# Performance work log

Hardware: AMD Instinct MI355X
Metric: run time of the kernel (lower is better)

Reference implementation:

```python
import jax, jax.numpy as jnp
import numpy as np

N_CODES = 1024
DIM = 64
COMMITMENT = 0.25


def setup_inputs() -> dict:
    key = jax.random.key(0)
    k1, k2 = jax.random.split(key)
    z = jax.random.normal(k1, (32, DIM, 64, 64), dtype=jnp.float32)  # [B, C, H, W]
    codebook = jax.random.uniform(
        k2, (N_CODES, DIM), dtype=jnp.float32,
        minval=-1.0 / N_CODES, maxval=1.0 / N_CODES,
    )
    return {"z": z, "codebook": codebook}


def reference(z, codebook):
    B, C, H, W = z.shape
    # [B, C, H, W] -> [B*H*W, C]
    z_flat = jnp.transpose(z, (0, 2, 3, 1)).reshape(-1, C)
    # Pairwise squared distances: ||z||^2 + ||e||^2 - 2 z.e  -> [N, n_codes]
    dists = (
        jnp.sum(z_flat * z_flat, axis=1, keepdims=True)
        + jnp.sum(codebook * codebook, axis=1)
        - 2.0 * (z_flat @ codebook.T)
    )
    indices = jnp.argmin(dists, axis=1)  # [N]
    z_q = codebook[indices].reshape(B, H, W, C).transpose(0, 3, 1, 2)  # [B, C, H, W]

    commit_loss = jnp.mean((jax.lax.stop_gradient(z_q) - z) ** 2)
    codebook_loss = jnp.mean((z_q - jax.lax.stop_gradient(z)) ** 2)
    vq_loss = codebook_loss + COMMITMENT * commit_loss

    # Straight-through estimator
    z_q_st = z + jax.lax.stop_gradient(z_q - z)

    # Codebook usage fraction (jit-friendly equivalent of len(unique)/n_codes)
    counts = jnp.zeros((codebook.shape[0],), dtype=jnp.int32).at[indices].add(1)
    usage = jnp.mean((counts > 0).astype(jnp.float32))

    return z_q_st, vq_loss, usage, indices.reshape(B, H, W)
```

## Files before the change

kernel.cpp:

```cpp
#include <hip/hip_runtime.h>

#define NCODES 1024
#define DIM 64
#define HW 4096
#define CHW 262144
#define NPOS 131072
#define NELEM 8388608
#define TAU 4e-5f

#define WS_LOSS 0
#define WS_CNT 4
#define WS_FLAGS 256
#define WS_BSWZ 8192
#define WS_CBN 270336
#define WS_LIST 274432

typedef __attribute__((ext_vector_type(8))) short bf16x8;
typedef __attribute__((ext_vector_type(4))) float f32x4;
typedef __attribute__((ext_vector_type(4))) unsigned int u32x4;

__device__ __forceinline__ unsigned short f2bf(float x) {
  unsigned u = __float_as_uint(x);
  return (unsigned short)((u + 0x7FFFu + ((u >> 16) & 1u)) >> 16);
}
__device__ __forceinline__ float bf2f(unsigned short h) {
  return __uint_as_float(((unsigned)h) << 16);
}
__device__ __forceinline__ unsigned fxf(float d) {
  unsigned u = __float_as_uint(d);
  return (u & 0x80000000u) ? ~u : (u | 0x80000000u);
}

__global__ __launch_bounds__(256) void vq_prep(const float* __restrict__ cb,
                                               unsigned short* __restrict__ bswz,
                                               float* __restrict__ cbn) {
  int t = blockIdx.x * 256 + threadIdx.x;
  int n = t >> 6, k = t & 63;
  float v = cb[n * 64 + k];
  unsigned short h = f2bf(v);
  unsigned short lo = f2bf(v - bf2f(h));
  int i = n >> 4, lmod = n & 15;
  int q = k >> 5, kr = k & 31;
  int e = ((kr >> 4) << 2) | (kr & 3);
  int l = lmod | (((kr >> 2) & 3) << 4);
  bswz[(((i * 2 + 0) * 2 + q) * 64 + l) * 8 + e] = h;
  bswz[(((i * 2 + 1) * 2 + q) * 64 + l) * 8 + e] = lo;
  if (k == 0) {
    const float* ep = cb + n * 64;
    float s = 0.f;
#pragma unroll
    for (int c = 0; c < 64; ++c) s = fmaf(ep[c], ep[c], s);
    cbn[n] = s;
  }
}

__global__ __launch_bounds__(512, 4) void vq_phaseA(
    const float* __restrict__ z, const float* __restrict__ cb,
    const unsigned short* __restrict__ bswz, const float* __restrict__ cbn,
    float* __restrict__ out_zq, float* __restrict__ out_idx,
    float* __restrict__ loss, unsigned* __restrict__ cnt,
    unsigned* __restrict__ list, int* __restrict__ flags) {
  const int tid = threadIdx.x, w = tid >> 6, l = tid & 63;
  const int l15 = l & 15, lg = (l >> 4) & 3;
  const int posbase = blockIdx.x * 256;
  const int b = posbase >> 12;
  const int hwb = posbase & 4095;

  bf16x8 A[2][2][2];
#pragma unroll
  for (int s = 0; s < 2; ++s) {
    const float* zp = z + (size_t)b * CHW + (hwb + w * 32 + s * 16 + l15);
#pragma unroll
    for (int q = 0; q < 2; ++q) {
      bf16x8 ah, al;
#pragma unroll
      for (int e = 0; e < 8; ++e) {
        int c = q * 32 + ((e >> 2) << 4) + (lg << 2) + (e & 3);
        float v = zp[c * HW];
        unsigned short h = f2bf(v);
        ah[e] = (short)h;
        al[e] = (short)f2bf(v - bf2f(h));
      }
      A[s][q][0] = ah;
      A[s][q][1] = al;
    }
  }

  float bd[2][4], b2[2][4];
  unsigned bi[2][4];
#pragma unroll
  for (int s = 0; s < 2; ++s)
#pragma unroll
    for (int r = 0; r < 4; ++r) {
      bd[s][r] = 3.4e38f; b2[s][r] = 3.4e38f; bi[s][r] = 0;
    }

  const u32x4* B = (const u32x4*)bswz;
  for (int i = 0; i < 64; ++i) {
    bf16x8 b00 = __builtin_bit_cast(bf16x8, B[(i * 4 + 0) * 64 + l]);
    bf16x8 b01 = __builtin_bit_cast(bf16x8, B[(i * 4 + 1) * 64 + l]);
    bf16x8 b10 = __builtin_bit_cast(bf16x8, B[(i * 4 + 2) * 64 + l]);
    bf16x8 b11 = __builtin_bit_cast(bf16x8, B[(i * 4 + 3) * 64 + l]);
    float cbnv = cbn[i * 16 + l15];
    unsigned nb = (unsigned)(i * 16 + l15);
#pragma unroll
    for (int s = 0; s < 2; ++s) {
      f32x4 C = {0.f, 0.f, 0.f, 0.f};
      C = __builtin_amdgcn_mfma_f32_16x16x32_bf16(A[s][0][0], b00, C, 0, 0, 0);
      C = __builtin_amdgcn_mfma_f32_16x16x32_bf16(A[s][1][0], b01, C, 0, 0, 0);
      C = __builtin_amdgcn_mfma_f32_16x16x32_bf16(A[s][0][0], b10, C, 0, 0, 0);
      C = __builtin_amdgcn_mfma_f32_16x16x32_bf16(A[s][1][0], b11, C, 0, 0, 0);
      C = __builtin_amdgcn_mfma_f32_16x16x32_bf16(A[s][0][1], b00, C, 0, 0, 0);
      C = __builtin_amdgcn_mfma_f32_16x16x32_bf16(A[s][1][1], b01, C, 0, 0, 0);
#pragma unroll
      for (int r = 0; r < 4; ++r) {
        float d = fmaf(C[r], -2.0f, cbnv);
        bool lt = d < bd[s][r];
        float loser = lt ? bd[s][r] : d;
        b2[s][r] = fminf(b2[s][r], loser);
        bd[s][r] = fminf(bd[s][r], d);
        bi[s][r] = lt ? nb : bi[s][r];
      }
    }
  }

  __shared__ unsigned res[256];
#pragma unroll
  for (int s = 0; s < 2; ++s)
#pragma unroll
    for (int r = 0; r < 4; ++r) {
      float d = bd[s][r], s2 = b2[s][r];
      unsigned idx = bi[s][r];
#pragma unroll
      for (int st = 1; st < 16; st <<= 1) {
        float od = __shfl_xor(d, st, 64);
        unsigned oi = __shfl_xor(idx, st, 64);
        float o2 = __shfl_xor(s2, st, 64);
        bool take = (od < d) || (od == d && oi < idx);
        float loser = take ? d : od;
        s2 = fminf(fminf(s2, o2), loser);
        d = take ? od : d;
        idx = take ? oi : idx;
      }
      if (l15 == 0) {
        float gap = s2 - d;
        res[w * 32 + s * 16 + lg * 4 + r] =
            idx | ((gap <= TAU) ? 0x80000000u : 0u);
      }
    }
  __syncthreads();

  const int pl = tid & 255, half = tid >> 8;
  unsigned pk = res[pl];
  unsigned bj = pk & 1023u;
  int pos = posbase + pl;
  float lsum = 0.f;
  if (pk & 0x80000000u) {
    if (half == 0) {
      unsigned idx = atomicAdd(cnt, 1u);
      list[idx] = (unsigned)pos;
    }
  } else {
    if (half == 0) {
      out_idx[pos] = (float)bj;
      flags[bj] = 1;
    }
    const float* zp = z + (size_t)b * CHW + (pos & 4095);
    const float* eb = cb + bj * 64;
    float* op = out_zq + (size_t)b * CHW + (pos & 4095);
#pragma unroll
    for (int cc = 0; cc < 32; ++cc) {
      int c = half * 32 + cc;
      float zv = zp[c * HW];
      float e = eb[c];
      float diff = e - zv;
      lsum = fmaf(diff, diff, lsum);
      op[c * HW] = zv + diff;
    }
  }
  for (int off = 32; off; off >>= 1) lsum += __shfl_down(lsum, off, 64);
  __shared__ float wsum[8];
  if (l == 0) wsum[w] = lsum;
  __syncthreads();
  if (tid == 0) {
    float t2 = 0.f;
#pragma unroll
    for (int i2 = 0; i2 < 8; ++i2) t2 += wsum[i2];
    atomicAdd(loss, t2);
  }
}

template <int W>
__device__ __forceinline__ void epilogue8(const float* __restrict__ eb,
                                          const float zr[DIM],
                                          float* __restrict__ op,
                                          float& lsum) {
#pragma unroll
  for (int cc = 0; cc < 8; ++cc) {
    const int c = W * 8 + cc;
    float e = eb[c];
    float diff = e - zr[c];
    lsum = fmaf(diff, diff, lsum);
    op[c * HW] = zr[c] + diff;
  }
}

__global__ __launch_bounds__(512, 2) void vq_phaseB(
    const float* __restrict__ z, const float* __restrict__ cb,
    const float* __restrict__ cbn, float* __restrict__ out_zq,
    float* __restrict__ out_idx, float* __restrict__ loss,
    const unsigned* __restrict__ cnt, const unsigned* __restrict__ list,
    int* __restrict__ flags) {
  const unsigned total = *cnt;
  const int t = threadIdx.x, w = t >> 6, l = t & 63;
  __shared__ unsigned long long keys[8][64];
  __shared__ float wsum[8];

  for (unsigned base = blockIdx.x * 64u; base < total; base += 2048u * 64u) {
    const bool active = (base + (unsigned)l) < total;
    const int pos = active ? (int)list[base + l] : 0;
    const int b = pos >> 12, hw = pos & 4095;
    const float* zp = z + (size_t)b * CHW + hw;

    float zr[DIM];
#pragma unroll
    for (int c = 0; c < DIM; ++c) zr[c] = zp[c * HW];
    float A = 0.f;
#pragma unroll
    for (int c = 0; c < DIM; ++c) A = fmaf(zr[c], zr[c], A);

    const int j0 = __builtin_amdgcn_readfirstlane(w * 128);
    float best = 3.4e38f;
    int bestj = j0;
    for (int jj = 0; jj < 128; ++jj) {
      const int j = j0 + jj;
      const float* ej = cb + j * 64;
      float d0 = 0.f, d1 = 0.f, d2 = 0.f, d3 = 0.f;
#pragma unroll
      for (int k = 0; k < 64; k += 4) {
        d0 = fmaf(zr[k + 0], ej[k + 0], d0);
        d1 = fmaf(zr[k + 1], ej[k + 1], d1);
        d2 = fmaf(zr[k + 2], ej[k + 2], d2);
        d3 = fmaf(zr[k + 3], ej[k + 3], d3);
      }
      float dot = (d0 + d1) + (d2 + d3);
      float dist = (A + cbn[j]) - 2.0f * dot;
      if (dist < best) { best = dist; bestj = j; }
    }

    __syncthreads();
    keys[w][l] = ((unsigned long long)fxf(best) << 32) | (unsigned)bestj;
    __syncthreads();
    unsigned long long km = keys[0][l];
#pragma unroll
    for (int ww = 1; ww < 8; ++ww) {
      unsigned long long k2 = keys[ww][l];
      km = km < k2 ? km : k2;
    }
    const unsigned bj = (unsigned)(km & 0xFFFFFFFFull);

    float lsum = 0.f;
    if (active) {
      const float* eb = cb + bj * 64;
      float* op = out_zq + (size_t)b * CHW + hw;
      if (w == 0)      epilogue8<0>(eb, zr, op, lsum);
      else if (w == 1) epilogue8<1>(eb, zr, op, lsum);
      else if (w == 2) epilogue8<2>(eb, zr, op, lsum);
      else if (w == 3) epilogue8<3>(eb, zr, op, lsum);
      else if (w == 4) epilogue8<4>(eb, zr, op, lsum);
      else if (w == 5) epilogue8<5>(eb, zr, op, lsum);
      else if (w == 6) epilogue8<6>(eb, zr, op, lsum);
      else             epilogue8<7>(eb, zr, op, lsum);
      if (w == 0) {
        out_idx[pos] = (float)bj;
        flags[bj] = 1;
      }
    }
    for (int off = 32; off; off >>= 1) lsum += __shfl_down(lsum, off, 64);
    if (l == 0) wsum[w] = lsum;
    __syncthreads();
    if (t == 0) {
      float t2 = 0.f;
#pragma unroll
      for (int i2 = 0; i2 < 8; ++i2) t2 += wsum[i2];
      atomicAdd(loss, t2);
    }
  }
}

__global__ __launch_bounds__(1024) void vq_finalize(
    const int* __restrict__ flags, const float* __restrict__ loss,
    float* __restrict__ out_scalars) {
  __shared__ int cnt_[16];
  int t = threadIdx.x;
  int f = flags[t];
  for (int off = 32; off; off >>= 1) f += __shfl_down(f, off, 64);
  int lane = t & 63, wid = t >> 6;
  if (lane == 0) cnt_[wid] = f;
  __syncthreads();
  if (t == 0) {
    int c = 0;
#pragma unroll
    for (int i = 0; i < 16; ++i) c += cnt_[i];
    out_scalars[0] = 1.25f * (*loss) / (float)NELEM;
    out_scalars[1] = (float)c / (float)NCODES;
  }
}

extern "C" void kernel_launch(void* const* d_in, const int* in_sizes, int n_in,
                              void* d_out, int out_size, void* d_ws, size_t ws_size,
                              hipStream_t stream) {
  const float* z = (const float*)d_in[0];
  const float* cb = (const float*)d_in[1];
  float* out = (float*)d_out;

  char* ws = (char*)d_ws;
  float* loss = (float*)(ws + WS_LOSS);
  unsigned* cnt = (unsigned*)(ws + WS_CNT);
  int* flags = (int*)(ws + WS_FLAGS);
  unsigned short* bswz = (unsigned short*)(ws + WS_BSWZ);
  float* cbn = (float*)(ws + WS_CBN);
  unsigned* list = (unsigned*)(ws + WS_LIST);

  hipMemsetAsync(d_ws, 0, 8192, stream);
  vq_prep<<<256, 256, 0, stream>>>(cb, bswz, cbn);
  vq_phaseA<<<512, 512, 0, stream>>>(z, cb, bswz, cbn, out, out + NELEM + 2,
                                     loss, cnt, list, flags);
  vq_phaseB<<<2048, 512, 0, stream>>>(z, cb, cbn, out, out + NELEM + 2, loss,
                                      cnt, list, flags);
  vq_finalize<<<1, NCODES, 0, stream>>>(flags, loss, out + NELEM);
}
```

Before: 219.1 us.

## Halve per-wave tile in VQ phase A, split MFMA chains, fold memset into prep

Phase A now has each wave handle 16 positions instead of 32, and the launch doubles to 1024 blocks with a higher occupancy bound. The six dependent MFMAs are split into three independent accumulator chains to shorten the dependency latency. The workspace memset is folded into the prep kernel, which removes one launch. Phase B's grid shrinks to 512 blocks and its codebook loop gets unroll 2. In exchange, each codebook tile loaded from memory is reused across fewer positions, so codebook traffic per position goes up.

```diff
diff --git a/kernel.cpp b/kernel.cpp
--- a/kernel.cpp
+++ b/kernel.cpp
@@ -33,8 +33,10 @@
 
 __global__ __launch_bounds__(256) void vq_prep(const float* __restrict__ cb,
                                                unsigned short* __restrict__ bswz,
-                                               float* __restrict__ cbn) {
+                                               float* __restrict__ cbn,
+                                               unsigned* __restrict__ wszero) {
   int t = blockIdx.x * 256 + threadIdx.x;
+  if (t < 2048) wszero[t] = 0u;
   int n = t >> 6, k = t & 63;
   float v = cb[n * 64 + k];
   unsigned short h = f2bf(v);
@@ -54,7 +56,7 @@
   }
 }
 
-__global__ __launch_bounds__(512, 4) void vq_phaseA(
+__global__ __launch_bounds__(512, 8) void vq_phaseA(
     const float* __restrict__ z, const float* __restrict__ cb,
     const unsigned short* __restrict__ bswz, const float* __restrict__ cbn,
     float* __restrict__ out_zq, float* __restrict__ out_idx,
@@ -62,14 +64,13 @@
     unsigned* __restrict__ list, int* __restrict__ flags) {
   const int tid = threadIdx.x, w = tid >> 6, l = tid & 63;
   const int l15 = l & 15, lg = (l >> 4) & 3;
-  const int posbase = blockIdx.x * 256;
+  const int posbase = blockIdx.x * 128;
   const int b = posbase >> 12;
   const int hwb = posbase & 4095;
 
-  bf16x8 A[2][2][2];
-#pragma unroll
-  for (int s = 0; s < 2; ++s) {
-    const float* zp = z + (size_t)b * CHW + (hwb + w * 32 + s * 16 + l15);
+  bf16x8 Ah[2], Al[2];
+  {
+    const float* zp = z + (size_t)b * CHW + (hwb + w * 16 + l15);
 #pragma unroll
     for (int q = 0; q < 2; ++q) {
       bf16x8 ah, al;
@@ -81,19 +82,15 @@
         ah[e] = (short)h;
         al[e] = (short)f2bf(v - bf2f(h));
       }
-      A[s][q][0] = ah;
-      A[s][q][1] = al;
-    }
-  }
-
-  float bd[2][4], b2[2][4];
-  unsigned bi[2][4];
-#pragma unroll
-  for (int s = 0; s < 2; ++s)
-#pragma unroll
-    for (int r = 0; r < 4; ++r) {
-      bd[s][r] = 3.4e38f; b2[s][r] = 3.4e38f; bi[s][r] = 0;
-    }
+      Ah[q] = ah;
+      Al[q] = al;
+    }
+  }
+
+  float bd[4], b2[4];
+  unsigned bi[4];
+#pragma unroll
+  for (int r = 0; r < 4; ++r) { bd[r] = 3.4e38f; b2[r] = 3.4e38f; bi[r] = 0; }
 
   const u32x4* B = (const u32x4*)bswz;
   for (int i = 0; i < 64; ++i) {
@@ -103,65 +100,60 @@
     bf16x8 b11 = __builtin_bit_cast(bf16x8, B[(i * 4 + 3) * 64 + l]);
     float cbnv = cbn[i * 16 + l15];
     unsigned nb = (unsigned)(i * 16 + l15);
-#pragma unroll
-    for (int s = 0; s < 2; ++s) {
-      f32x4 C = {0.f, 0.f, 0.f, 0.f};
-      C = __builtin_amdgcn_mfma_f32_16x16x32_bf16(A[s][0][0], b00, C, 0, 0, 0);
-      C = __builtin_amdgcn_mfma_f32_16x16x32_bf16(A[s][1][0], b01, C, 0, 0, 0);
-      C = __builtin_amdgcn_mfma_f32_16x16x32_bf16(A[s][0][0], b10, C, 0, 0, 0);
-      C = __builtin_amdgcn_mfma_f32_16x16x32_bf16(A[s][1][0], b11, C, 0, 0, 0);
-      C = __builtin_amdgcn_mfma_f32_16x16x32_bf16(A[s][0][1], b00, C, 0, 0, 0);
-      C = __builtin_amdgcn_mfma_f32_16x16x32_bf16(A[s][1][1], b01, C, 0, 0, 0);
-#pragma unroll
-      for (int r = 0; r < 4; ++r) {
-        float d = fmaf(C[r], -2.0f, cbnv);
-        bool lt = d < bd[s][r];
-        float loser = lt ? bd[s][r] : d;
-        b2[s][r] = fminf(b2[s][r], loser);
-        bd[s][r] = fminf(bd[s][r], d);
-        bi[s][r] = lt ? nb : bi[s][r];
-      }
-    }
-  }
-
-  __shared__ unsigned res[256];
-#pragma unroll
-  for (int s = 0; s < 2; ++s)
+    f32x4 Ca = {0.f, 0.f, 0.f, 0.f};
+    f32x4 Cb = {0.f, 0.f, 0.f, 0.f};
+    f32x4 Cc = {0.f, 0.f, 0.f, 0.f};
+    Ca = __builtin_amdgcn_mfma_f32_16x16x32_bf16(Ah[0], b00, Ca, 0, 0, 0);
+    Cb = __builtin_amdgcn_mfma_f32_16x16x32_bf16(Ah[0], b10, Cb, 0, 0, 0);
+    Cc = __builtin_amdgcn_mfma_f32_16x16x32_bf16(Al[0], b00, Cc, 0, 0, 0);
+    Ca = __builtin_amdgcn_mfma_f32_16x16x32_bf16(Ah[1], b01, Ca, 0, 0, 0);
+    Cb = __builtin_amdgcn_mfma_f32_16x16x32_bf16(Ah[1], b11, Cb, 0, 0, 0);
+    Cc = __builtin_amdgcn_mfma_f32_16x16x32_bf16(Al[1], b01, Cc, 0, 0, 0);
 #pragma unroll
     for (int r = 0; r < 4; ++r) {
-      float d = bd[s][r], s2 = b2[s][r];
-      unsigned idx = bi[s][r];
-#pragma unroll
-      for (int st = 1; st < 16; st <<= 1) {
-        float od = __shfl_xor(d, st, 64);
-        unsigned oi = __shfl_xor(idx, st, 64);
-        float o2 = __shfl_xor(s2, st, 64);
-        bool take = (od < d) || (od == d && oi < idx);
-        float loser = take ? d : od;
-        s2 = fminf(fminf(s2, o2), loser);
-        d = take ? od : d;
-        idx = take ? oi : idx;
-      }
-      if (l15 == 0) {
-        float gap = s2 - d;
-        res[w * 32 + s * 16 + lg * 4 + r] =
-            idx | ((gap <= TAU) ? 0x80000000u : 0u);
-      }
-    }
+      float d = fmaf(Ca[r] + (Cb[r] + Cc[r]), -2.0f, cbnv);
+      bool lt = d < bd[r];
+      float loser = lt ? bd[r] : d;
+      b2[r] = fminf(b2[r], loser);
+      bd[r] = fminf(bd[r], d);
+      bi[r] = lt ? nb : bi[r];
+    }
+  }
+
+  __shared__ unsigned res[128];
+#pragma unroll
+  for (int r = 0; r < 4; ++r) {
+    float d = bd[r], s2 = b2[r];
+    unsigned idx = bi[r];
+#pragma unroll
+    for (int st = 1; st < 16; st <<= 1) {
+      float od = __shfl_xor(d, st, 64);
+      unsigned oi = __shfl_xor(idx, st, 64);
+      float o2 = __shfl_xor(s2, st, 64);
+      bool take = (od < d) || (od == d && oi < idx);
+      float loser = take ? d : od;
+      s2 = fminf(fminf(s2, o2), loser);
+      d = take ? od : d;
+      idx = take ? oi : idx;
+    }
+    if (l15 == 0) {
+      res[w * 16 + lg * 4 + r] = idx | (((s2 - d) <= TAU) ? 0x80000000u : 0u);
+    }
+  }
   __syncthreads();
 
-  const int pl = tid & 255, half = tid >> 8;
+  const int pl = tid & 127, quarter = tid >> 7;
   unsigned pk = res[pl];
   unsigned bj = pk & 1023u;
   int pos = posbase + pl;
   float lsum = 0.f;
   if (pk & 0x80000000u) {
-    if (half == 0) {
+    if (quarter == 0) {
       unsigned idx = atomicAdd(cnt, 1u);
       list[idx] = (unsigned)pos;
     }
   } else {
-    if (half == 0) {
+    if (quarter == 0) {
       out_idx[pos] = (float)bj;
       flags[bj] = 1;
     }
@@ -169,8 +161,8 @@
     const float* eb = cb + bj * 64;
     float* op = out_zq + (size_t)b * CHW + (pos & 4095);
 #pragma unroll
-    for (int cc = 0; cc < 32; ++cc) {
-      int c = half * 32 + cc;
+    for (int cc = 0; cc < 16; ++cc) {
+      int c = quarter * 16 + cc;
       float zv = zp[c * HW];
       float e = eb[c];
       float diff = e - zv;
@@ -216,7 +208,7 @@
   __shared__ unsigned long long keys[8][64];
   __shared__ float wsum[8];
 
-  for (unsigned base = blockIdx.x * 64u; base < total; base += 2048u * 64u) {
+  for (unsigned base = blockIdx.x * 64u; base < total; base += 512u * 64u) {
     const bool active = (base + (unsigned)l) < total;
     const int pos = active ? (int)list[base + l] : 0;
     const int b = pos >> 12, hw = pos & 4095;
@@ -232,6 +224,7 @@
     const int j0 = __builtin_amdgcn_readfirstlane(w * 128);
     float best = 3.4e38f;
     int bestj = j0;
+#pragma unroll 2
     for (int jj = 0; jj < 128; ++jj) {
       const int j = j0 + jj;
       const float* ej = cb + j * 64;
@@ -322,11 +315,10 @@
   float* cbn = (float*)(ws + WS_CBN);
   unsigned* list = (unsigned*)(ws + WS_LIST);
 
-  hipMemsetAsync(d_ws, 0, 8192, stream);
-  vq_prep<<<256, 256, 0, stream>>>(cb, bswz, cbn);
-  vq_phaseA<<<512, 512, 0, stream>>>(z, cb, bswz, cbn, out, out + NELEM + 2,
-                                     loss, cnt, list, flags);
-  vq_phaseB<<<2048, 512, 0, stream>>>(z, cb, cbn, out, out + NELEM + 2, loss,
-                                      cnt, list, flags);
+  vq_prep<<<256, 256, 0, stream>>>(cb, bswz, cbn, (unsigned*)d_ws);
+  vq_phaseA<<<1024, 512, 0, stream>>>(z, cb, bswz, cbn, out, out + NELEM + 2,
+                                      loss, cnt, list, flags);
+  vq_phaseB<<<512, 512, 0, stream>>>(z, cb, cbn, out, out + NELEM + 2, loss,
+                                     cnt, list, flags);
   vq_finalize<<<1, NCODES, 0, stream>>>(flags, loss, out + NELEM);
 }
```

Result: no change. 221.4 us (+1.1%).
